# Performance work log

Measured on AMD Instinct MI355X. Metric: run time of the kernel, lower is better.

Reference implementation:

```python
import jax, jax.numpy as jnp
import numpy as np

N_IN = 512
N_OUT = 256
K = 3
GRID_SIZE = N_OUT - K + 1  # 254
X_LO, X_HI = -1.0, 1.0
BATCH = 1024
LN_EPS = 1e-5


def make_grid():
    # grid_values: (n_in, grid_size + 2k + 1), identical rows as in the torch module
    step = (X_HI - X_LO) / GRID_SIZE
    g = jnp.linspace(X_LO - step * K, X_HI + step * K, GRID_SIZE + 2 * K + 1, dtype=jnp.float32)
    return jnp.broadcast_to(g, (N_IN, g.shape[0]))


def setup_inputs() -> dict:
    key = jax.random.key(0)
    k1, k2, k3 = jax.random.split(key, 3)
    x = jax.random.normal(k1, (BATCH, N_IN), dtype=jnp.float32)
    # kaiming-uniform-like scale for the linear weights
    weights = jax.random.normal(k2, (N_OUT, N_IN), dtype=jnp.float32) * (1.0 / np.sqrt(N_IN))
    spline_weights = jax.random.normal(k3, (N_OUT, N_IN, GRID_SIZE + K), dtype=jnp.float32) * (
        1.0 / np.sqrt(N_IN * (GRID_SIZE + K))
    )
    prelu_a = jnp.full((1,), 0.25, dtype=jnp.float32)  # PReLU default init
    return {"x": x, "weights": weights, "spline_weights": spline_weights, "prelu_a": prelu_a}


def reference(x, weights, spline_weights, prelu_a):
    g = make_grid()  # (n_in, P) with P = GRID_SIZE + 2K + 1
    # base branch: tanh(x) @ W^T
    b_out = jnp.tanh(x) @ weights.T  # (B, n_out)

    # Cox-de Boor recursion for B-spline bases
    xe = x[:, :, None]  # (B, n_in, 1)
    bases = ((xe >= g[:, :-1]) & (xe < g[:, 1:])).astype(x.dtype)  # (B, n_in, P-1)
    for k in range(1, K + 1):
        left = g[:, : -(k + 1)]
        right = g[:, k:-1]
        delta = jnp.where(right == left, jnp.ones_like(right), right - left)
        bases = (xe - left) / delta * bases[:, :, :-1] + (
            (g[:, k + 1 :] - xe) / (g[:, k + 1 :] - g[:, 1:-k])
        ) * bases[:, :, 1:]
    # bases: (B, n_in, GRID_SIZE + K)

    # flattened linear == einsum over (n_in, grid) axes
    spline_out = jnp.einsum("big,oig->bo", bases, spline_weights)  # (B, n_out)

    y = b_out + spline_out
    # LayerNorm without affine params
    mu = jnp.mean(y, axis=-1, keepdims=True)
    var = jnp.var(y, axis=-1, keepdims=True)
    yn = (y - mu) / jnp.sqrt(var + LN_EPS)
    # PReLU (single shared slope)
    return jnp.where(yn >= 0, yn, prelu_a[0] * yn)
```

## Files before the change

kernel.cpp:

```cpp
#include <hip/hip_runtime.h>
#include <math.h>

#define N_IN   512
#define N_OUT  256
#define NCOEF  257
#define BATCH  1024
#define LN_EPS 1e-5f

#define OC 16
#define IG 32
#define BC 512

#define STEPF (2.0f/254.0f)
#define G0F   (-1.0f - 3.0f*STEPF)


__global__ __launch_bounds__(256, 2) void kan_main(
    const float* __restrict__ x, const float* __restrict__ W,
    const float* __restrict__ sw, float* __restrict__ part)
{
    const int bid = blockIdx.x;
    const int oc = bid & 15;
    const int ig = (bid >> 4) & 15;
    const int bc = bid >> 8;
    const int o0 = oc * OC;
    const int i0 = ig * IG;
    const int b0 = bc * BC;
    const int t  = threadIdx.x;

    __shared__ __align__(16) float slab[NCOEF * 16];
    __shared__ float4 wls[BC];
    __shared__ float2 txpb[BC];
    __shared__ __align__(16) float Wl[OC];

    const int wv  = t >> 6;
    const int bl  = (t >> 2) & 15;
    const int og  = t & 3;
    const int lbb = wv * 128;

    const int soo  = t >> 4;
    const int scb  = t & 15;
    const int colp = soo ^ (((scb >> 2) & 3) << 2);

    float4 acc[8];
#pragma unroll
    for (int bp = 0; bp < 8; ++bp) acc[bp] = make_float4(0.f, 0.f, 0.f, 0.f);

    for (int ii = 0; ii < IG; ++ii) {
        const int i = i0 + ii;
        __syncthreads();

#pragma unroll
        for (int r = 0; r < 2; ++r) {
            const int lb = t + r * 256;
            const float xv = x[(size_t)(b0 + lb) * N_IN + i];
            const float e2 = __expf(2.f * xv);
            const float tx = 1.f - 2.f / (e2 + 1.f);
            const float u  = (xv - G0F) * 127.f;
            const bool has = (u >= 0.f) && (u < 260.f);
            const float uf = has ? u : 0.f;
            int m = (int)uf;
            if (m > 259) m = 259;
            const float tt = uf - (float)m;
            const float t2 = tt * tt, t3 = t2 * tt;
            const float omt = 1.f - tt;
            float a0 = omt * omt * omt * (1.f / 6.f);
            float a1 = (3.f * t3 - 6.f * t2 + 4.f) * (1.f / 6.f);
            float a2 = (-3.f * t3 + 3.f * t2 + 3.f * tt + 1.f) * (1.f / 6.f);
            float a3 = t3 * (1.f / 6.f);
            if (!has) { a0 = a1 = a2 = a3 = 0.f; }
            const int pb = m - 3;
            const int pbc = pb < 0 ? 0 : (pb > 253 ? 253 : pb);
            const int d = pbc - pb;
            if (d >= 1)  { a0 = a1; a1 = a2; a2 = a3; a3 = 0.f; }
            if (d >= 2)  { a0 = a1; a1 = a2; a2 = a3; a3 = 0.f; }
            if (d >= 3)  { a0 = a1; a1 = a2; a2 = a3; a3 = 0.f; }
            if (d <= -1) { a3 = a2; a2 = a1; a1 = a0; a0 = 0.f; }
            if (d <= -2) { a3 = a2; a2 = a1; a1 = a0; a0 = 0.f; }
            if (d <= -3) { a3 = a2; a2 = a1; a1 = a0; a0 = 0.f; }
            wls[lb]  = make_float4(a0, a1, a2, a3);
            txpb[lb] = make_float2(tx, (float)pbc);
        }

        if (t < OC) Wl[t] = W[(size_t)(o0 + t) * N_IN + i];

        {
            const float* rp = sw + ((size_t)(o0 + soo) * N_IN + i) * NCOEF;
#pragma unroll
            for (int e = 0; e < 4; ++e) {
                const int c0 = e * 64 + scb * 4;
                const float v0 = rp[c0 + 0], v1 = rp[c0 + 1];
                const float v2 = rp[c0 + 2], v3 = rp[c0 + 3];
                float* wp = &slab[(c0 << 4) + colp];
                wp[0]  = v0;
                wp[16] = v1;
                wp[32] = v2;
                wp[48] = v3;
            }
            if (scb == 15) slab[(256 << 4) + soo] = rp[256];
        }
        __syncthreads();

        const float4 Wv = *reinterpret_cast<const float4*>(&Wl[og << 2]);

#pragma unroll
        for (int bp = 0; bp < 8; ++bp) {
            const int lb = lbb + bp * 16 + bl;
            const float4 w4 = wls[lb];
            const float2 tp = txpb[lb];
            const int pb = (int)tp.y;
            float4 a = acc[bp];
            a.x += tp.x * Wv.x; a.y += tp.x * Wv.y;
            a.z += tp.x * Wv.z; a.w += tp.x * Wv.w;
#pragma unroll
            for (int k = 0; k < 4; ++k) {
                const int p = pb + k;
                const int cidx = (p << 4) + ((og ^ ((p >> 4) & 3)) << 2);
                const float4 s4 = *reinterpret_cast<const float4*>(&slab[cidx]);
                const float wk = (k == 0) ? w4.x : (k == 1) ? w4.y
                               : (k == 2) ? w4.z : w4.w;
                a.x += wk * s4.x; a.y += wk * s4.y;
                a.z += wk * s4.z; a.w += wk * s4.w;
            }
            acc[bp] = a;
        }
    }

    float* dst = part + ((size_t)ig * BATCH + b0) * N_OUT + o0 + (og << 2);
#pragma unroll
    for (int bp = 0; bp < 8; ++bp) {
        const int lb = lbb + bp * 16 + bl;
        *reinterpret_cast<float4*>(&dst[(size_t)lb * N_OUT]) = acc[bp];
    }
}

__global__ __launch_bounds__(256) void kan_ln(
    const float* __restrict__ part, const float* __restrict__ prelu_a,
    float* __restrict__ out)
{
    const int b = blockIdx.x;
    const int t = threadIdx.x;

    float s = 0.f;
#pragma unroll
    for (int k = 0; k < 16; ++k)
        s += part[((size_t)k * BATCH + b) * N_OUT + t];

    float v1 = s, v2 = s * s;
#pragma unroll
    for (int d = 1; d < 64; d <<= 1) {
        v1 += __shfl_xor(v1, d);
        v2 += __shfl_xor(v2, d);
    }
    __shared__ float r1[4], r2[4];
    if ((t & 63) == 0) { r1[t >> 6] = v1; r2[t >> 6] = v2; }
    __syncthreads();
    const float tot1 = r1[0] + r1[1] + r1[2] + r1[3];
    const float tot2 = r2[0] + r2[1] + r2[2] + r2[3];

    const float mu  = tot1 * (1.f / N_OUT);
    const float var = tot2 * (1.f / N_OUT) - mu * mu;
    const float inv = rsqrtf(var + LN_EPS);
    const float yn  = (s - mu) * inv;
    const float a   = prelu_a[0];
    out[(size_t)b * N_OUT + t] = (yn >= 0.f) ? yn : a * yn;
}

extern "C" void kernel_launch(void* const* d_in, const int* in_sizes, int n_in,
                              void* d_out, int out_size, void* d_ws, size_t ws_size,
                              hipStream_t stream)
{
    const float* x  = (const float*)d_in[0];
    const float* W  = (const float*)d_in[1];
    const float* sw = (const float*)d_in[2];
    const float* pa = (const float*)d_in[3];
    float* out  = (float*)d_out;
    float* part = (float*)d_ws;

    kan_main<<<dim3(512), 256, 0, stream>>>(x, W, sw, part);
    kan_ln<<<dim3(1024), 256, 0, stream>>>(part, pa, out);
}
```

Measured before the change: 111.5 us.

## Halve batch chunk, prefetch next slab in registers, pack spline weights bf16

Batch chunk per block drops from 512 to 256, so the grid doubles to 1024 blocks with launch bounds raised to 4 blocks per CU. Spline weights, x and W for the next input column are now loaded into registers while the current column is computed, overlapping global loads with the inner accumulate loop. Per-sample basis weights are packed as bf16 pairs into one uint4 alongside tanh and the index, and samples with all-zero bases skip the slab reads. This trades precision of the basis weights and doubles re-reads of the spline weight slab for better latency hiding and occupancy.

```diff
diff --git a/kernel.cpp b/kernel.cpp
--- a/kernel.cpp
+++ b/kernel.cpp
@@ -9,13 +9,18 @@
 
 #define OC 16
 #define IG 32
-#define BC 512
-
-#define STEPF (2.0f/254.0f)
-#define G0F   (-1.0f - 3.0f*STEPF)
-
-
-__global__ __launch_bounds__(256, 2) void kan_main(
+#define BC 256
+
+#define G0F (-1.0f - 3.0f * (2.0f / 254.0f))
+
+
+static __device__ __forceinline__ unsigned pk_bf16x2(float a, float b) {
+    unsigned ua = ((__float_as_uint(a) + 0x8000u) >> 16) & 0xffffu;
+    unsigned ub = (__float_as_uint(b) + 0x8000u) & 0xffff0000u;
+    return ua | ub;
+}
+
+__global__ __launch_bounds__(256, 4) void kan_main(
     const float* __restrict__ x, const float* __restrict__ W,
     const float* __restrict__ sw, float* __restrict__ part)
 {
@@ -23,37 +28,40 @@
     const int oc = bid & 15;
     const int ig = (bid >> 4) & 15;
     const int bc = bid >> 8;
-    const int o0 = oc * OC;
-    const int i0 = ig * IG;
-    const int b0 = bc * BC;
-    const int t  = threadIdx.x;
+    const int o0 = oc * OC, i0 = ig * IG, b0 = bc * BC;
+    const int t = threadIdx.x;
 
     __shared__ __align__(16) float slab[NCOEF * 16];
-    __shared__ float4 wls[BC];
-    __shared__ float2 txpb[BC];
+    __shared__ __align__(16) uint4 wpk[BC];
     __shared__ __align__(16) float Wl[OC];
 
-    const int wv  = t >> 6;
-    const int bl  = (t >> 2) & 15;
-    const int og  = t & 3;
-    const int lbb = wv * 128;
-
-    const int soo  = t >> 4;
-    const int scb  = t & 15;
+    const int wv = t >> 6, bl = (t >> 2) & 15, og = t & 3;
+    const int soo = t >> 4, scb = t & 15;
     const int colp = soo ^ (((scb >> 2) & 3) << 2);
 
-    float4 acc[8];
-#pragma unroll
-    for (int bp = 0; bp < 8; ++bp) acc[bp] = make_float4(0.f, 0.f, 0.f, 0.f);
+    const float* rp  = sw + ((size_t)(o0 + soo) * N_IN + i0) * NCOEF;
+    const float* xp  = x + (size_t)(b0 + t) * N_IN + i0;
+    const float* wgp = W + (size_t)(o0 + (t & 15)) * N_IN + i0;
+
+    float pf[16], pfT, xcur, Wcur;
+#pragma unroll
+    for (int e = 0; e < 4; ++e) {
+        const int c0 = e * 64 + scb * 4;
+        pf[e * 4 + 0] = rp[c0 + 0]; pf[e * 4 + 1] = rp[c0 + 1];
+        pf[e * 4 + 2] = rp[c0 + 2]; pf[e * 4 + 3] = rp[c0 + 3];
+    }
+    pfT  = (scb == 15) ? rp[256] : 0.f;
+    xcur = xp[0];
+    Wcur = (t < OC) ? wgp[0] : 0.f;
+
+    float4 acc[4];
+#pragma unroll
+    for (int bp = 0; bp < 4; ++bp) acc[bp] = make_float4(0.f, 0.f, 0.f, 0.f);
 
     for (int ii = 0; ii < IG; ++ii) {
-        const int i = i0 + ii;
-        __syncthreads();
-
-#pragma unroll
-        for (int r = 0; r < 2; ++r) {
-            const int lb = t + r * 256;
-            const float xv = x[(size_t)(b0 + lb) * N_IN + i];
+        uint4 wp;
+        {
+            const float xv = xcur;
             const float e2 = __expf(2.f * xv);
             const float tx = 1.f - 2.f / (e2 + 1.f);
             const float u  = (xv - G0F) * 127.f;
@@ -69,58 +77,75 @@
             float a2 = (-3.f * t3 + 3.f * t2 + 3.f * tt + 1.f) * (1.f / 6.f);
             float a3 = t3 * (1.f / 6.f);
             if (!has) { a0 = a1 = a2 = a3 = 0.f; }
-            const int pb = m - 3;
+            const int pb  = m - 3;
             const int pbc = pb < 0 ? 0 : (pb > 253 ? 253 : pb);
-            const int d = pbc - pb;
+            const int d   = pbc - pb;
             if (d >= 1)  { a0 = a1; a1 = a2; a2 = a3; a3 = 0.f; }
             if (d >= 2)  { a0 = a1; a1 = a2; a2 = a3; a3 = 0.f; }
             if (d >= 3)  { a0 = a1; a1 = a2; a2 = a3; a3 = 0.f; }
             if (d <= -1) { a3 = a2; a2 = a1; a1 = a0; a0 = 0.f; }
             if (d <= -2) { a3 = a2; a2 = a1; a1 = a0; a0 = 0.f; }
             if (d <= -3) { a3 = a2; a2 = a1; a1 = a0; a0 = 0.f; }
-            wls[lb]  = make_float4(a0, a1, a2, a3);
-            txpb[lb] = make_float2(tx, (float)pbc);
-        }
-
-        if (t < OC) Wl[t] = W[(size_t)(o0 + t) * N_IN + i];
-
-        {
-            const float* rp = sw + ((size_t)(o0 + soo) * N_IN + i) * NCOEF;
+            wp.x = pk_bf16x2(a0, a1);
+            wp.y = pk_bf16x2(a2, a3);
+            wp.z = __float_as_uint(tx);
+            wp.w = (unsigned)pbc;
+        }
+
+        __syncthreads();
+
+#pragma unroll
+        for (int e = 0; e < 4; ++e) {
+            const int c0 = e * 64 + scb * 4;
+            float* wpt = &slab[(c0 << 4) + colp];
+            wpt[0]  = pf[e * 4 + 0];
+            wpt[16] = pf[e * 4 + 1];
+            wpt[32] = pf[e * 4 + 2];
+            wpt[48] = pf[e * 4 + 3];
+        }
+        if (scb == 15) slab[(256 << 4) + soo] = pfT;
+        wpk[t] = wp;
+        if (t < OC) Wl[t] = Wcur;
+        __syncthreads();
+
+        if (ii + 1 < IG) {
+            rp += NCOEF;
 #pragma unroll
             for (int e = 0; e < 4; ++e) {
                 const int c0 = e * 64 + scb * 4;
-                const float v0 = rp[c0 + 0], v1 = rp[c0 + 1];
-                const float v2 = rp[c0 + 2], v3 = rp[c0 + 3];
-                float* wp = &slab[(c0 << 4) + colp];
-                wp[0]  = v0;
-                wp[16] = v1;
-                wp[32] = v2;
-                wp[48] = v3;
+                pf[e * 4 + 0] = rp[c0 + 0]; pf[e * 4 + 1] = rp[c0 + 1];
+                pf[e * 4 + 2] = rp[c0 + 2]; pf[e * 4 + 3] = rp[c0 + 3];
             }
-            if (scb == 15) slab[(256 << 4) + soo] = rp[256];
-        }
-        __syncthreads();
+            pfT  = (scb == 15) ? rp[256] : 0.f;
+            xcur = xp[ii + 1];
+            if (t < OC) Wcur = wgp[ii + 1];
+        }
 
         const float4 Wv = *reinterpret_cast<const float4*>(&Wl[og << 2]);
-
-#pragma unroll
-        for (int bp = 0; bp < 8; ++bp) {
-            const int lb = lbb + bp * 16 + bl;
-            const float4 w4 = wls[lb];
-            const float2 tp = txpb[lb];
-            const int pb = (int)tp.y;
+#pragma unroll
+        for (int bp = 0; bp < 4; ++bp) {
+            const int lb = wv * 64 + bp * 16 + bl;
+            const uint4 u = wpk[lb];
+            const float tx = __uint_as_float(u.z);
             float4 a = acc[bp];
-            a.x += tp.x * Wv.x; a.y += tp.x * Wv.y;
-            a.z += tp.x * Wv.z; a.w += tp.x * Wv.w;
-#pragma unroll
-            for (int k = 0; k < 4; ++k) {
-                const int p = pb + k;
-                const int cidx = (p << 4) + ((og ^ ((p >> 4) & 3)) << 2);
-                const float4 s4 = *reinterpret_cast<const float4*>(&slab[cidx]);
-                const float wk = (k == 0) ? w4.x : (k == 1) ? w4.y
-                               : (k == 2) ? w4.z : w4.w;
-                a.x += wk * s4.x; a.y += wk * s4.y;
-                a.z += wk * s4.z; a.w += wk * s4.w;
+            a.x += tx * Wv.x; a.y += tx * Wv.y;
+            a.z += tx * Wv.z; a.w += tx * Wv.w;
+            if (u.x | u.y) {
+                const int pb = (int)u.w;
+                const float w0 = __uint_as_float(u.x << 16);
+                const float w1 = __uint_as_float(u.x & 0xffff0000u);
+                const float w2 = __uint_as_float(u.y << 16);
+                const float w3 = __uint_as_float(u.y & 0xffff0000u);
+#pragma unroll
+                for (int k = 0; k < 4; ++k) {
+                    const int p = pb + k;
+                    const int cidx = (p << 4) + ((og ^ ((p >> 4) & 3)) << 2);
+                    const float4 s4 = *reinterpret_cast<const float4*>(&slab[cidx]);
+                    const float wk = (k == 0) ? w0 : (k == 1) ? w1
+                                   : (k == 2) ? w2 : w3;
+                    a.x += wk * s4.x; a.y += wk * s4.y;
+                    a.z += wk * s4.z; a.w += wk * s4.w;
+                }
             }
             acc[bp] = a;
         }
@@ -128,8 +153,8 @@
 
     float* dst = part + ((size_t)ig * BATCH + b0) * N_OUT + o0 + (og << 2);
 #pragma unroll
-    for (int bp = 0; bp < 8; ++bp) {
-        const int lb = lbb + bp * 16 + bl;
+    for (int bp = 0; bp < 4; ++bp) {
+        const int lb = wv * 64 + bp * 16 + bl;
         *reinterpret_cast<float4*>(&dst[(size_t)lb * N_OUT]) = acc[bp];
     }
 }
@@ -177,6 +202,6 @@
     float* out  = (float*)d_out;
     float* part = (float*)d_ws;
 
-    kan_main<<<dim3(512), 256, 0, stream>>>(x, W, sw, part);
+    kan_main<<<dim3(1024), 256, 0, stream>>>(x, W, sw, part);
     kan_ln<<<dim3(1024), 256, 0, stream>>>(part, pa, out);
 }
```

Result: slower. 159.9 us (+43.4%).
